# Kernel optimization log

Measured on AMD Instinct MI355X. Metric: run time of the kernel, lower is better.

The kernel has to match this reference:

```python
import jax, jax.numpy as jnp
import numpy as np

N, M, D_IN, D_OUT = 8192, 8192, 512, 512


def setup_inputs() -> dict:
    key = jax.random.key(0)
    k1, k2, k3, k4 = jax.random.split(key, 4)
    return {
        "x": jax.random.normal(k1, (N, D_OUT), dtype=jnp.float32),
        "mu": jax.random.normal(k2, (M, D_IN), dtype=jnp.float32),
        "W": jax.random.normal(k3, (D_OUT, D_IN), dtype=jnp.float32),
        "b": jax.random.normal(k4, (D_OUT,), dtype=jnp.float32),
    }


def reference(x, mu, W, b):
    # f_mu: (M, D_out) -- projection + nonlinearity (func = tanh)
    f_mu = jnp.tanh(mu @ W.T + b)
    # measure m[n, m] = -0.5 * ||x_n - f_mu_m||^2, via the matmul expansion
    # (avoids the (N, M, D) diff tensor; same math as sum of squared diffs)
    x_sq = jnp.sum(x * x, axis=-1)            # (N,)
    f_sq = jnp.sum(f_mu * f_mu, axis=-1)      # (M,)
    cross = x @ f_mu.T                        # (N, M)
    m = -0.5 * (x_sq[:, None] - 2.0 * cross + f_sq[None, :])
    # energy: -sum over rows of logsumexp over axis 1
    return -jnp.sum(jax.nn.logsumexp(m, axis=1))
```

## Files before the change

### kernel.cpp

```cpp
#include <hip/hip_runtime.h>

#define D 512
#define NROWS 8192
#define MROWS 8192
#define NCHUNK 8
#define CHUNK_COLS (MROWS / NCHUNK)
#define SWEEPS (CHUNK_COLS / 256)
#define NRB (NROWS / 128)
#define LOG2E 1.4426950408889634f
#define LN2 0.6931471805599453f

typedef float floatx4 __attribute__((ext_vector_type(4)));
typedef __bf16 bf16x8 __attribute__((ext_vector_type(8)));
typedef unsigned uintx4 __attribute__((ext_vector_type(4)));

typedef __attribute__((address_space(1))) void* as1_void_p;
typedef __attribute__((address_space(3))) void* as3_void_p;

__device__ __forceinline__ void async_cp16(const void* g, void* l) {
    __builtin_amdgcn_global_load_lds((as1_void_p)(void*)g, (as3_void_p)l, 16, 0, 0);
}

__device__ __forceinline__ unsigned short f2bf(float f) {
    unsigned u = __float_as_uint(f);
    u += 0x7fffu + ((u >> 16) & 1u);
    return (unsigned short)(u >> 16);
}
__device__ __forceinline__ float bf2f(unsigned short h) {
    return __uint_as_float(((unsigned)h) << 16);
}

__device__ __forceinline__ float fast_tanh(float x) {
    const float xc = fminf(fmaxf(x, -15.0f), 15.0f);
    const float e = __builtin_exp2f(xc * (2.0f * LOG2E));
    return (e - 1.0f) * __builtin_amdgcn_rcpf(e + 1.0f);
}

__device__ __forceinline__ unsigned pack2(float a, float b) {
    return (unsigned)f2bf(a) | ((unsigned)f2bf(b) << 16);
}

#define XBLK (NROWS / 4)
#define MUBLK (MROWS * D / 2048)
#define WBLK (D * D / 2048)
__global__ void k_prep(const float* __restrict__ x,
                       const float* __restrict__ mu,
                       const float* __restrict__ W,
                       unsigned short* __restrict__ xb,
                       unsigned short* __restrict__ mub,
                       unsigned short* __restrict__ Wb,
                       float* __restrict__ xsq,
                       float* __restrict__ fsq,
                       float* __restrict__ out) {
    const int bid = blockIdx.x;
    const int t = threadIdx.x;
    if (bid < XBLK) {
        if (bid == 0 && t == 0) out[0] = 0.f;
        const int row = bid * 4 + (t >> 6);
        const int lane = t & 63;
        const float4 v0 = ((const float4*)(x + (size_t)row * D))[lane * 2];
        const float4 v1 = ((const float4*)(x + (size_t)row * D))[lane * 2 + 1];
        uintx4 o;
        o.x = pack2(v0.x * LOG2E, v0.y * LOG2E);
        o.y = pack2(v0.z * LOG2E, v0.w * LOG2E);
        o.z = pack2(v1.x * LOG2E, v1.y * LOG2E);
        o.w = pack2(v1.z * LOG2E, v1.w * LOG2E);
        ((uintx4*)(xb + (size_t)row * D))[lane] = o;
        float s = v0.x * v0.x + v0.y * v0.y + v0.z * v0.z + v0.w * v0.w
                + v1.x * v1.x + v1.y * v1.y + v1.z * v1.z + v1.w * v1.w;
        #pragma unroll
        for (int m = 1; m < 64; m <<= 1) s += __shfl_xor(s, m);
        if (lane == 0) xsq[row] = s;
    } else if (bid < XBLK + MUBLK) {
        const size_t i = ((size_t)(bid - XBLK) * 256 + t) * 2;
        const float4 v0 = ((const float4*)mu)[i];
        const float4 v1 = ((const float4*)mu)[i + 1];
        uintx4 o;
        o.x = pack2(v0.x, v0.y); o.y = pack2(v0.z, v0.w);
        o.z = pack2(v1.x, v1.y); o.w = pack2(v1.z, v1.w);
        ((uintx4*)mub)[i / 2] = o;
    } else {
        const int wb = bid - XBLK - MUBLK;
        const size_t i = ((size_t)wb * 256 + t) * 2;
        const float4 v0 = ((const float4*)W)[i];
        const float4 v1 = ((const float4*)W)[i + 1];
        uintx4 o;
        o.x = pack2(v0.x, v0.y); o.y = pack2(v0.z, v0.w);
        o.z = pack2(v1.x, v1.y); o.w = pack2(v1.z, v1.w);
        ((uintx4*)Wb)[i / 2] = o;
        if (t < 64) fsq[wb * 64 + t] = 0.f;
    }
}

__global__ __launch_bounds__(256, 2)
void k_fgemm(const unsigned short* __restrict__ mub,
             const unsigned short* __restrict__ Wb,
             const float* __restrict__ bias,
             unsigned short* __restrict__ fb,
             float* __restrict__ fsq) {
    __shared__ unsigned short Ab[128 * 32];
    __shared__ unsigned short Bb[64 * 32];

    const int tid = threadIdx.x;
    const int wave = tid >> 6;
    const int lane = tid & 63;
    const int wr = wave >> 1, wc = wave & 1;
    const int g = lane >> 4;
    const int lm = lane & 15;

    const int row0 = blockIdx.x * 128;
    const int col0 = blockIdx.y * 64;

    const int srow = tid >> 2;
    const int gsrc = (tid & 3) ^ ((srow >> 1) & 3);
    const unsigned short* gA = mub + (size_t)(row0 + srow) * D + gsrc * 8;
    const unsigned short* gB = Wb  + (size_t)(col0 + srow) * D + gsrc * 8;
    char* lA = ((char*)Ab) + wave * 1024;
    char* lB = ((char*)Bb) + wave * 1024;

    const int xsel = (lm >> 1) & 3;
    const unsigned short* fragA = Ab + (64 * wr + lm) * 32 + (g ^ xsel) * 8;
    const unsigned short* fragB = Bb + (32 * wc + lm) * 32 + (g ^ xsel) * 8;

    floatx4 acc[4][2];
    const floatx4 zz = {0.f, 0.f, 0.f, 0.f};
    #pragma unroll
    for (int i = 0; i < 4; ++i)
        #pragma unroll
        for (int j = 0; j < 2; ++j) acc[i][j] = zz;

    for (int kt = 0; kt < 16; ++kt) {
        const int k0 = kt * 32;
        async_cp16(gA + k0, lA);
        async_cp16(gA + 64 * D + k0, lA + 4096);
        async_cp16(gB + k0, lB);
        __syncthreads();
        bf16x8 af[4], bfr[2];
        #pragma unroll
        for (int i = 0; i < 4; ++i) af[i] = *(const bf16x8*)(fragA + i * 512);
        #pragma unroll
        for (int j = 0; j < 2; ++j) bfr[j] = *(const bf16x8*)(fragB + j * 512);
        #pragma unroll
        for (int i = 0; i < 4; ++i)
            #pragma unroll
            for (int j = 0; j < 2; ++j)
                acc[i][j] = __builtin_amdgcn_mfma_f32_16x16x32_bf16(af[i], bfr[j], acc[i][j], 0, 0, 0);
        __syncthreads();
    }

    float bcol[2];
    #pragma unroll
    for (int j = 0; j < 2; ++j) bcol[j] = bias[col0 + 32 * wc + 16 * j + lm];
    #pragma unroll
    for (int i = 0; i < 4; ++i) {
        #pragma unroll
        for (int r = 0; r < 4; ++r) {
            const int row = row0 + 64 * wr + 16 * i + 4 * g + r;
            float sq = 0.f;
            #pragma unroll
            for (int j = 0; j < 2; ++j) {
                const int col = col0 + 32 * wc + 16 * j + lm;
                const unsigned short h = f2bf(fast_tanh(acc[i][j][r] + bcol[j]));
                fb[(size_t)row * D + col] = h;
                const float fr = bf2f(h);
                sq += fr * fr;
            }
            #pragma unroll
            for (int d = 1; d < 16; d <<= 1) sq += __shfl_xor(sq, d);
            if (lm == 0) atomicAdd(fsq + row, sq);
        }
    }
}

__global__ __launch_bounds__(256, 2)
void k_cross(const unsigned short* __restrict__ xb,
             const unsigned short* __restrict__ fb,
             const float* __restrict__ fsq,
             float* __restrict__ pmax,
             float* __restrict__ psum) {
    __shared__ unsigned short Ab[2][128 * 32];
    __shared__ unsigned short Bb[2][256 * 32];
    __shared__ float mbuf[128], sbuf[128];

    const int tid = threadIdx.x;
    const int wave = tid >> 6;
    const int lane = tid & 63;
    const int wr = wave >> 1, wc = wave & 1;
    const int g = lane >> 4;
    const int lm = lane & 15;

    const int row0 = blockIdx.x * 128;
    const int chunk = blockIdx.y;

    const int srow = tid >> 2;
    const int gsrc = (tid & 3) ^ ((srow >> 1) & 3);
    const unsigned short* gA = xb + (size_t)(row0 + srow) * D + gsrc * 8;
    char* lA0 = ((char*)Ab[0]) + wave * 1024;
    char* lA1 = ((char*)Ab[1]) + wave * 1024;
    char* lB0 = ((char*)Bb[0]) + wave * 1024;
    char* lB1 = ((char*)Bb[1]) + wave * 1024;

    const int xsel = (lm >> 1) & 3;
    const unsigned short* fragA0 = Ab[0] + (64 * wr + lm) * 32 + (g ^ xsel) * 8;
    const unsigned short* fragB0 = Bb[0] + (128 * wc + lm) * 32 + (g ^ xsel) * 8;

    float m_loc[4][4], s_loc[4][4];
    #pragma unroll
    for (int i = 0; i < 4; ++i)
        #pragma unroll
        for (int r = 0; r < 4; ++r) { m_loc[i][r] = -__builtin_inff(); s_loc[i][r] = 0.f; }

    for (int st = 0; st < SWEEPS; ++st) {
        const int col0 = chunk * CHUNK_COLS + st * 256;
        const unsigned short* gB = fb + (size_t)(col0 + srow) * D + gsrc * 8;

        floatx4 acc[4][8];
        const floatx4 zz = {0.f, 0.f, 0.f, 0.f};
        #pragma unroll
        for (int i = 0; i < 4; ++i)
            #pragma unroll
            for (int j = 0; j < 8; ++j) acc[i][j] = zz;

        for (int kt = 0; kt < 8; ++kt) {
            const int k0 = kt * 64;
            async_cp16(gA + k0, lA0);
            async_cp16(gA + 64 * D + k0, lA0 + 4096);
            async_cp16(gA + k0 + 32, lA1);
            async_cp16(gA + 64 * D + k0 + 32, lA1 + 4096);
            #pragma unroll
            for (int h = 0; h < 4; ++h) {
                async_cp16(gB + (size_t)(64 * h) * D + k0, lB0 + 4096 * h);
                async_cp16(gB + (size_t)(64 * h) * D + k0 + 32, lB1 + 4096 * h);
            }
            __syncthreads();
            #pragma unroll
            for (int h = 0; h < 2; ++h) {
                const unsigned short* fA = fragA0 + h * 4096;
                const unsigned short* fB = fragB0 + h * 8192;
                bf16x8 af[4];
                #pragma unroll
                for (int i = 0; i < 4; ++i) af[i] = *(const bf16x8*)(fA + i * 512);
                #pragma unroll
                for (int j = 0; j < 8; ++j) {
                    const bf16x8 bj = *(const bf16x8*)(fB + j * 512);
                    acc[0][j] = __builtin_amdgcn_mfma_f32_16x16x32_bf16(af[0], bj, acc[0][j], 0, 0, 0);
                    acc[1][j] = __builtin_amdgcn_mfma_f32_16x16x32_bf16(af[1], bj, acc[1][j], 0, 0, 0);
                    acc[2][j] = __builtin_amdgcn_mfma_f32_16x16x32_bf16(af[2], bj, acc[2][j], 0, 0, 0);
                    acc[3][j] = __builtin_amdgcn_mfma_f32_16x16x32_bf16(af[3], bj, acc[3][j], 0, 0, 0);
                }
            }
            __syncthreads();
        }

        float hf[8];
        #pragma unroll
        for (int j = 0; j < 8; ++j)
            hf[j] = 0.5f * LOG2E * fsq[col0 + 128 * wc + 16 * j + lm];
        #pragma unroll
        for (int i = 0; i < 4; ++i) {
            #pragma unroll
            for (int r = 0; r < 4; ++r) {
                float v[8];
                float mm = -__builtin_inff();
                #pragma unroll
                for (int j = 0; j < 8; ++j) {
                    v[j] = acc[i][j][r] - hf[j];
                    mm = fmaxf(mm, v[j]);
                }
                const float nm = fmaxf(m_loc[i][r], mm);
                float s = s_loc[i][r] * __builtin_exp2f(m_loc[i][r] - nm);
                #pragma unroll
                for (int j = 0; j < 8; ++j) s += __builtin_exp2f(v[j] - nm);
                s_loc[i][r] = s;
                m_loc[i][r] = nm;
            }
        }
    }

    #pragma unroll
    for (int i = 0; i < 4; ++i) {
        #pragma unroll
        for (int r = 0; r < 4; ++r) {
            float m = m_loc[i][r], s = s_loc[i][r];
            #pragma unroll
            for (int d = 1; d < 16; d <<= 1) {
                const float om = __shfl_xor(m, d);
                const float os = __shfl_xor(s, d);
                const float nm = fmaxf(m, om);
                s = s * __builtin_exp2f(m - nm) + os * __builtin_exp2f(om - nm);
                m = nm;
            }
            m_loc[i][r] = m; s_loc[i][r] = s;
        }
    }
    if (wc == 0 && lm == 0) {
        #pragma unroll
        for (int i = 0; i < 4; ++i)
            #pragma unroll
            for (int r = 0; r < 4; ++r) {
                const int rl = 64 * wr + 16 * i + 4 * g + r;
                mbuf[rl] = m_loc[i][r]; sbuf[rl] = s_loc[i][r];
            }
    }
    __syncthreads();
    if (wc == 1 && lm == 0) {
        #pragma unroll
        for (int i = 0; i < 4; ++i)
            #pragma unroll
            for (int r = 0; r < 4; ++r) {
                const int rl = 64 * wr + 16 * i + 4 * g + r;
                const float om = mbuf[rl], os = sbuf[rl];
                float m = m_loc[i][r], s = s_loc[i][r];
                const float nm = fmaxf(m, om);
                s = s * __builtin_exp2f(m - nm) + os * __builtin_exp2f(om - nm);
                pmax[(size_t)(row0 + rl) * NCHUNK + chunk] = nm;
                psum[(size_t)(row0 + rl) * NCHUNK + chunk] = s;
            }
    }
}

__global__ void k_finish(const float* __restrict__ pmax,
                         const float* __restrict__ psum,
                         const float* __restrict__ xsq,
                         float* __restrict__ out) {
    const int row = blockIdx.x * 256 + threadIdx.x;
    const float4* pm4 = (const float4*)(pmax + (size_t)row * NCHUNK);
    const float4* ps4 = (const float4*)(psum + (size_t)row * NCHUNK);
    float pm[NCHUNK], ps[NCHUNK];
    #pragma unroll
    for (int c = 0; c < NCHUNK / 4; ++c) {
        const float4 a = pm4[c], b = ps4[c];
        pm[4*c] = a.x; pm[4*c+1] = a.y; pm[4*c+2] = a.z; pm[4*c+3] = a.w;
        ps[4*c] = b.x; ps[4*c+1] = b.y; ps[4*c+2] = b.z; ps[4*c+3] = b.w;
    }
    float gm = -__builtin_inff();
    #pragma unroll
    for (int c = 0; c < NCHUNK; ++c) gm = fmaxf(gm, pm[c]);
    float s = 0.f;
    #pragma unroll
    for (int c = 0; c < NCHUNK; ++c) s += ps[c] * __builtin_exp2f(pm[c] - gm);
    float lse = LN2 * (gm + __builtin_log2f(s)) - 0.5f * xsq[row];
    #pragma unroll
    for (int m = 1; m < 64; m <<= 1) lse += __shfl_xor(lse, m);
    __shared__ float ws4[4];
    if ((threadIdx.x & 63) == 0) ws4[threadIdx.x >> 6] = lse;
    __syncthreads();
    if (threadIdx.x == 0) atomicAdd(out, -(ws4[0] + ws4[1] + ws4[2] + ws4[3]));
}

extern "C" void kernel_launch(void* const* d_in, const int* in_sizes, int n_in,
                              void* d_out, int out_size, void* d_ws, size_t ws_size,
                              hipStream_t stream) {
    const float* x  = (const float*)d_in[0];
    const float* mu = (const float*)d_in[1];
    const float* W  = (const float*)d_in[2];
    const float* b  = (const float*)d_in[3];

    char* ws = (char*)d_ws;
    unsigned short* xb  = (unsigned short*)(ws);
    unsigned short* fb  = (unsigned short*)(ws + (8u << 20));
    unsigned short* mub = (unsigned short*)(ws + (16u << 20));
    unsigned short* Wb  = (unsigned short*)(ws + (24u << 20));
    float* xsq  = (float*)(ws + (25u << 20));
    float* fsq  = xsq + NROWS;
    float* pmax = fsq + MROWS;
    float* psum = pmax + (size_t)NROWS * NCHUNK;

    float* out = (float*)d_out;

    hipLaunchKernelGGL(k_prep, dim3(XBLK + MUBLK + WBLK), dim3(256), 0, stream,
                       x, mu, W, xb, mub, Wb, xsq, fsq, out);
    hipLaunchKernelGGL(k_fgemm, dim3(MROWS / 128, D / 64), dim3(256), 0, stream,
                       mub, Wb, b, fb, fsq);
    hipLaunchKernelGGL(k_cross, dim3(NRB, NCHUNK), dim3(256), 0, stream,
                       xb, fb, fsq, pmax, psum);
    hipLaunchKernelGGL(k_finish, dim3(NROWS / 256), dim3(256), 0, stream,
                       pmax, psum, xsq, out);
}
```

Before: 172.4 us.

## Switch cross-term GEMM operands from bf16 to fp8 e4m3

Quantizes the log2e-scaled x and the tanh output f_mu to fp8 instead of bf16. The cross GEMM now uses fp8 MFMA (16x16x32 fp8_fp8) with half-size LDS tiles and half as many async global-to-LDS copies per k-step. Row norms are computed from the dequantized fp8 values, so the measure stays consistent with the quantized dot products, and the final x-norm term is rescaled by ln2^2. This cuts memory and LDS traffic and workspace size, but the coarse fp8 rounding may push the summed energy past the accuracy tolerance.

```diff
diff --git a/kernel.cpp b/kernel.cpp
--- a/kernel.cpp
+++ b/kernel.cpp
@@ -46,7 +46,7 @@
 __global__ void k_prep(const float* __restrict__ x,
                        const float* __restrict__ mu,
                        const float* __restrict__ W,
-                       unsigned short* __restrict__ xb,
+                       unsigned char* __restrict__ xb8,
                        unsigned short* __restrict__ mub,
                        unsigned short* __restrict__ Wb,
                        float* __restrict__ xsq,
@@ -60,14 +60,22 @@
         const int lane = t & 63;
         const float4 v0 = ((const float4*)(x + (size_t)row * D))[lane * 2];
         const float4 v1 = ((const float4*)(x + (size_t)row * D))[lane * 2 + 1];
-        uintx4 o;
-        o.x = pack2(v0.x * LOG2E, v0.y * LOG2E);
-        o.y = pack2(v0.z * LOG2E, v0.w * LOG2E);
-        o.z = pack2(v1.x * LOG2E, v1.y * LOG2E);
-        o.w = pack2(v1.z * LOG2E, v1.w * LOG2E);
-        ((uintx4*)(xb + (size_t)row * D))[lane] = o;
-        float s = v0.x * v0.x + v0.y * v0.y + v0.z * v0.z + v0.w * v0.w
-                + v1.x * v1.x + v1.y * v1.y + v1.z * v1.z + v1.w * v1.w;
+        int p0 = 0, p1 = 0;
+        p0 = __builtin_amdgcn_cvt_pk_fp8_f32(v0.x * LOG2E, v0.y * LOG2E, p0, false);
+        p0 = __builtin_amdgcn_cvt_pk_fp8_f32(v0.z * LOG2E, v0.w * LOG2E, p0, true);
+        p1 = __builtin_amdgcn_cvt_pk_fp8_f32(v1.x * LOG2E, v1.y * LOG2E, p1, false);
+        p1 = __builtin_amdgcn_cvt_pk_fp8_f32(v1.z * LOG2E, v1.w * LOG2E, p1, true);
+        uint2 o; o.x = (unsigned)p0; o.y = (unsigned)p1;
+        ((uint2*)(xb8 + (size_t)row * D))[lane] = o;
+        float q, s = 0.f;
+        q = __builtin_amdgcn_cvt_f32_fp8(p0, 0); s += q * q;
+        q = __builtin_amdgcn_cvt_f32_fp8(p0, 1); s += q * q;
+        q = __builtin_amdgcn_cvt_f32_fp8(p0, 2); s += q * q;
+        q = __builtin_amdgcn_cvt_f32_fp8(p0, 3); s += q * q;
+        q = __builtin_amdgcn_cvt_f32_fp8(p1, 0); s += q * q;
+        q = __builtin_amdgcn_cvt_f32_fp8(p1, 1); s += q * q;
+        q = __builtin_amdgcn_cvt_f32_fp8(p1, 2); s += q * q;
+        q = __builtin_amdgcn_cvt_f32_fp8(p1, 3); s += q * q;
         #pragma unroll
         for (int m = 1; m < 64; m <<= 1) s += __shfl_xor(s, m);
         if (lane == 0) xsq[row] = s;
@@ -96,7 +104,7 @@
 void k_fgemm(const unsigned short* __restrict__ mub,
              const unsigned short* __restrict__ Wb,
              const float* __restrict__ bias,
-             unsigned short* __restrict__ fb,
+             unsigned char* __restrict__ fb8,
              float* __restrict__ fsq) {
     __shared__ unsigned short Ab[128 * 32];
     __shared__ unsigned short Bb[64 * 32];
@@ -160,10 +168,11 @@
             #pragma unroll
             for (int j = 0; j < 2; ++j) {
                 const int col = col0 + 32 * wc + 16 * j + lm;
-                const unsigned short h = f2bf(fast_tanh(acc[i][j][r] + bcol[j]));
-                fb[(size_t)row * D + col] = h;
-                const float fr = bf2f(h);
-                sq += fr * fr;
+                const float tv = fast_tanh(acc[i][j][r] + bcol[j]);
+                const int pk = __builtin_amdgcn_cvt_pk_fp8_f32(tv, tv, 0, false);
+                fb8[(size_t)row * D + col] = (unsigned char)(pk & 0xff);
+                const float qf = __builtin_amdgcn_cvt_f32_fp8(pk, 0);
+                sq += qf * qf;
             }
             #pragma unroll
             for (int d = 1; d < 16; d <<= 1) sq += __shfl_xor(sq, d);
@@ -173,13 +182,13 @@
 }
 
 __global__ __launch_bounds__(256, 2)
-void k_cross(const unsigned short* __restrict__ xb,
-             const unsigned short* __restrict__ fb,
+void k_cross(const unsigned char* __restrict__ xb8,
+             const unsigned char* __restrict__ fb8,
              const float* __restrict__ fsq,
              float* __restrict__ pmax,
              float* __restrict__ psum) {
-    __shared__ unsigned short Ab[2][128 * 32];
-    __shared__ unsigned short Bb[2][256 * 32];
+    __shared__ char Ab[128 * 64];
+    __shared__ char Bb[256 * 64];
     __shared__ float mbuf[128], sbuf[128];
 
     const int tid = threadIdx.x;
@@ -193,16 +202,15 @@
     const int chunk = blockIdx.y;
 
     const int srow = tid >> 2;
-    const int gsrc = (tid & 3) ^ ((srow >> 1) & 3);
-    const unsigned short* gA = xb + (size_t)(row0 + srow) * D + gsrc * 8;
-    char* lA0 = ((char*)Ab[0]) + wave * 1024;
-    char* lA1 = ((char*)Ab[1]) + wave * 1024;
-    char* lB0 = ((char*)Bb[0]) + wave * 1024;
-    char* lB1 = ((char*)Bb[1]) + wave * 1024;
+    const int gsrc = ((tid & 3) ^ ((srow >> 1) & 3)) * 16;
+    const unsigned char* gA = xb8 + (size_t)(row0 + srow) * D + gsrc;
+    char* lA = Ab + wave * 1024;
+    char* lB = Bb + wave * 1024;
 
     const int xsel = (lm >> 1) & 3;
-    const unsigned short* fragA0 = Ab[0] + (64 * wr + lm) * 32 + (g ^ xsel) * 8;
-    const unsigned short* fragB0 = Bb[0] + (128 * wc + lm) * 32 + (g ^ xsel) * 8;
+    const char* fragA = Ab + (64 * wr + lm) * 64;
+    const char* fragB = Bb + (128 * wc + lm) * 64;
+    const int sub = (g & 1) * 8;
 
     float m_loc[4][4], s_loc[4][4];
     #pragma unroll
@@ -212,7 +220,7 @@
 
     for (int st = 0; st < SWEEPS; ++st) {
         const int col0 = chunk * CHUNK_COLS + st * 256;
-        const unsigned short* gB = fb + (size_t)(col0 + srow) * D + gsrc * 8;
+        const unsigned char* gB = fb8 + (size_t)(col0 + srow) * D + gsrc;
 
         floatx4 acc[4][8];
         const floatx4 zz = {0.f, 0.f, 0.f, 0.f};
@@ -223,30 +231,26 @@
 
         for (int kt = 0; kt < 8; ++kt) {
             const int k0 = kt * 64;
-            async_cp16(gA + k0, lA0);
-            async_cp16(gA + 64 * D + k0, lA0 + 4096);
-            async_cp16(gA + k0 + 32, lA1);
-            async_cp16(gA + 64 * D + k0 + 32, lA1 + 4096);
-            #pragma unroll
-            for (int h = 0; h < 4; ++h) {
-                async_cp16(gB + (size_t)(64 * h) * D + k0, lB0 + 4096 * h);
-                async_cp16(gB + (size_t)(64 * h) * D + k0 + 32, lB1 + 4096 * h);
-            }
+            async_cp16(gA + k0, lA);
+            async_cp16(gA + (size_t)64 * D + k0, lA + 4096);
+            #pragma unroll
+            for (int h4 = 0; h4 < 4; ++h4)
+                async_cp16(gB + (size_t)(64 * h4) * D + k0, lB + 4096 * h4);
             __syncthreads();
             #pragma unroll
             for (int h = 0; h < 2; ++h) {
-                const unsigned short* fA = fragA0 + h * 4096;
-                const unsigned short* fB = fragB0 + h * 8192;
-                bf16x8 af[4];
-                #pragma unroll
-                for (int i = 0; i < 4; ++i) af[i] = *(const bf16x8*)(fA + i * 512);
+                const int pg = ((h * 2 + (g >> 1)) ^ xsel) * 16 + sub;
+                long a0 = *(const long*)(fragA + 0 * 1024 + pg);
+                long a1 = *(const long*)(fragA + 1 * 1024 + pg);
+                long a2 = *(const long*)(fragA + 2 * 1024 + pg);
+                long a3 = *(const long*)(fragA + 3 * 1024 + pg);
                 #pragma unroll
                 for (int j = 0; j < 8; ++j) {
-                    const bf16x8 bj = *(const bf16x8*)(fB + j * 512);
-                    acc[0][j] = __builtin_amdgcn_mfma_f32_16x16x32_bf16(af[0], bj, acc[0][j], 0, 0, 0);
-                    acc[1][j] = __builtin_amdgcn_mfma_f32_16x16x32_bf16(af[1], bj, acc[1][j], 0, 0, 0);
-                    acc[2][j] = __builtin_amdgcn_mfma_f32_16x16x32_bf16(af[2], bj, acc[2][j], 0, 0, 0);
-                    acc[3][j] = __builtin_amdgcn_mfma_f32_16x16x32_bf16(af[3], bj, acc[3][j], 0, 0, 0);
+                    const long bj = *(const long*)(fragB + j * 1024 + pg);
+                    acc[0][j] = __builtin_amdgcn_mfma_f32_16x16x32_fp8_fp8(a0, bj, acc[0][j], 0, 0, 0);
+                    acc[1][j] = __builtin_amdgcn_mfma_f32_16x16x32_fp8_fp8(a1, bj, acc[1][j], 0, 0, 0);
+                    acc[2][j] = __builtin_amdgcn_mfma_f32_16x16x32_fp8_fp8(a2, bj, acc[2][j], 0, 0, 0);
+                    acc[3][j] = __builtin_amdgcn_mfma_f32_16x16x32_fp8_fp8(a3, bj, acc[3][j], 0, 0, 0);
                 }
             }
             __syncthreads();
@@ -339,7 +343,7 @@
     float s = 0.f;
     #pragma unroll
     for (int c = 0; c < NCHUNK; ++c) s += ps[c] * __builtin_exp2f(pm[c] - gm);
-    float lse = LN2 * (gm + __builtin_log2f(s)) - 0.5f * xsq[row];
+    float lse = LN2 * (gm + __builtin_log2f(s)) - 0.5f * (LN2 * LN2) * xsq[row];
     #pragma unroll
     for (int m = 1; m < 64; m <<= 1) lse += __shfl_xor(lse, m);
     __shared__ float ws4[4];
@@ -357,11 +361,11 @@
     const float* b  = (const float*)d_in[3];
 
     char* ws = (char*)d_ws;
-    unsigned short* xb  = (unsigned short*)(ws);
-    unsigned short* fb  = (unsigned short*)(ws + (8u << 20));
-    unsigned short* mub = (unsigned short*)(ws + (16u << 20));
-    unsigned short* Wb  = (unsigned short*)(ws + (24u << 20));
-    float* xsq  = (float*)(ws + (25u << 20));
+    unsigned char*  xb8 = (unsigned char*)(ws);
+    unsigned char*  fb8 = (unsigned char*)(ws + (4u << 20));
+    unsigned short* mub = (unsigned short*)(ws + (8u << 20));
+    unsigned short* Wb  = (unsigned short*)(ws + (16u << 20));
+    float* xsq  = (float*)(ws + (17u << 20));
     float* fsq  = xsq + NROWS;
     float* pmax = fsq + MROWS;
     float* psum = pmax + (size_t)NROWS * NCHUNK;
@@ -369,11 +373,11 @@
     float* out = (float*)d_out;
 
     hipLaunchKernelGGL(k_prep, dim3(XBLK + MUBLK + WBLK), dim3(256), 0, stream,
-                       x, mu, W, xb, mub, Wb, xsq, fsq, out);
+                       x, mu, W, xb8, mub, Wb, xsq, fsq, out);
     hipLaunchKernelGGL(k_fgemm, dim3(MROWS / 128, D / 64), dim3(256), 0, stream,
-                       mub, Wb, b, fb, fsq);
+                       mub, Wb, b, fb8, fsq);
     hipLaunchKernelGGL(k_cross, dim3(NRB, NCHUNK), dim3(256), 0, stream,
-                       xb, fb, fsq, pmax, psum);
+                       xb8, fb8, fsq, pmax, psum);
     hipLaunchKernelGGL(k_finish, dim3(NROWS / 256), dim3(256), 0, stream,
                        pmax, psum, xsq, out);
 }
```

After: 168.4 us. 1.02x faster.
